# Optimization experiments

Measured on AMD Instinct MI355X. Metric: run time of the kernel, lower is better.

The kernel has to match this reference:

```python
import jax, jax.numpy as jnp
import numpy as np

B, N, F, T, K, FO = 16, 1024, 64, 24, 3, 64


def setup_inputs() -> dict:
    key = jax.random.key(0)
    ks = jax.random.split(key, 8)
    sc = 0.05
    x = jax.random.normal(ks[0], (B, N, F, T), dtype=jnp.float32)
    W1 = jax.random.normal(ks[1], (T,), dtype=jnp.float32) * sc
    W2 = jax.random.normal(ks[2], (F, T), dtype=jnp.float32) * sc
    W3 = jax.random.normal(ks[3], (F,), dtype=jnp.float32) * sc
    bs = jax.random.normal(ks[4], (1, N, N), dtype=jnp.float32) * sc
    Vs = jax.random.normal(ks[5], (N, N), dtype=jnp.float32) * sc
    cheb = jax.random.normal(ks[6], (K, N, N), dtype=jnp.float32) * sc
    Theta = jax.random.normal(ks[7], (K, F, FO), dtype=jnp.float32) * sc
    return {"x": x, "W1": W1, "W2": W2, "W3": W3, "bs": bs, "Vs": Vs,
            "cheb": cheb, "Theta": Theta}


def spatial_attention(x, W1, W2, W3, bs, Vs):
    # x: (B,N,F,T) -> S: (B,N,N)
    lhs = jnp.einsum('bnft,t->bnf', x, W1)          # (B,N,F)
    lhs = jnp.einsum('bnf,ft->bnt', lhs, W2)        # (B,N,T)
    rhs = jnp.einsum('f,bnft->btn', W3, x)          # (B,T,N)
    product = jnp.einsum('bnt,btm->bnm', lhs, rhs)  # (B,N,N)
    S = jnp.einsum('ik,bkj->bij', Vs, jax.nn.sigmoid(product + bs))
    return jax.nn.softmax(S, axis=1)


def reference(x, W1, W2, W3, bs, Vs, cheb, Theta):
    # x: (B,N,F,T); cheb: (K,N,N); Theta: (K,F,FO)
    S = spatial_attention(x, W1, W2, W3, bs, Vs)    # (B,N,N)
    out = jnp.zeros((x.shape[0], x.shape[1], Theta.shape[2], x.shape[3]),
                    dtype=x.dtype)
    for k in range(cheb.shape[0]):                  # small fixed K
        Tat = cheb[k] * S                           # (B,N,N) attention-masked T_k
        # T_k_with_at.permute(0,2,1) @ graph_signal, vectorized over t
        r = jnp.einsum('bnm,bnft->bmft', Tat, x)    # (B,N,F,T)
        out = out + jnp.einsum('bmft,fo->bmot', r, Theta[k])
    return jax.nn.relu(out)                         # (B,N,FO,T)
```

## Files before the change

### kernel.cpp

```cpp
#include <hip/hip_runtime.h>
#include <math.h>

#define Bc 16
#define Nc 1024
#define Fc 64
#define Tc 24
#define Kc 3
#define FOc 64
#define Cc (Fc*Tc)
#define KKc (Kc*Nc)

typedef __attribute__((ext_vector_type(8))) short short8;
typedef __attribute__((ext_vector_type(8))) unsigned short u16x8;
typedef __attribute__((ext_vector_type(4))) float f32x4;

__device__ __forceinline__ unsigned short f2bf(float f) {
  unsigned u = __float_as_uint(f);
  u += 0x7fff + ((u >> 16) & 1);
  return (unsigned short)(u >> 16);
}
__device__ __forceinline__ float bf2f(unsigned short h) {
  return __uint_as_float((unsigned)h << 16);
}

#define GLL16(g, l) __builtin_amdgcn_global_load_lds( \
    (const __attribute__((address_space(1))) void*)(g), \
    (__attribute__((address_space(3))) void*)(l), 16, 0, 0)

__device__ __forceinline__ f32x4 mfma16(short8 a, short8 b, f32x4 c) {
  return __builtin_amdgcn_mfma_f32_16x16x32_bf16(a, b, c, 0, 0, 0);
}

__global__ __launch_bounds__(64) void prep_kernel(
    const float* __restrict__ x, const float* __restrict__ W1,
    const float* __restrict__ W2, const float* __restrict__ W3,
    float* __restrict__ lhs, float* __restrict__ rhs) {
  int bn = blockIdx.x;
  int tid = threadIdx.x;
  __shared__ float xs[Fc * 25];
  __shared__ float w1s[Tc];
  __shared__ float w3s[Fc];
  __shared__ float af[Fc];
  const float* xp = x + (size_t)bn * Cc;
  for (int i = tid; i < Cc; i += 64) xs[(i / Tc) * 25 + (i % Tc)] = xp[i];
  if (tid < Tc) w1s[tid] = W1[tid];
  w3s[tid] = W3[tid];
  __syncthreads();
  float a = 0.f;
  #pragma unroll
  for (int t = 0; t < Tc; ++t) a += xs[tid * 25 + t] * w1s[t];
  af[tid] = a;
  __syncthreads();
  if (tid < Tc) {
    float l = 0.f, r2 = 0.f;
    #pragma unroll 8
    for (int f = 0; f < Fc; ++f) {
      l  += af[f] * W2[f * Tc + tid];
      r2 += w3s[f] * xs[f * 25 + tid];
    }
    lhs[(size_t)bn * Tc + tid] = l;
    rhs[(size_t)bn * Tc + tid] = r2;
  }
}

__global__ __launch_bounds__(256) void prodsigT_kernel(
    const float* __restrict__ lhs, const float* __restrict__ rhs,
    const float* __restrict__ bs, unsigned short* __restrict__ sigT) {
  int b = blockIdx.z;
  int p0 = blockIdx.y * 64, q0 = blockIdx.x * 64;
  __shared__ float Ls[64 * 25], Rs[64 * 25], Bt[64 * 65];
  int tid = threadIdx.x;
  const float* lp = lhs + ((size_t)b * Nc + q0) * Tc;
  const float* rp = rhs + ((size_t)b * Nc + p0) * Tc;
  for (int i = tid; i < 64 * Tc; i += 256) {
    Ls[(i / Tc) * 25 + i % Tc] = lp[i];
    Rs[(i / Tc) * 25 + i % Tc] = rp[i];
  }
  for (int i = tid; i < 1024; i += 256) {
    int qr = i >> 4, pc = (i & 15) * 4;
    *(float4*)&Bt[qr * 65 + pc] = *(const float4*)&bs[(size_t)(q0 + qr) * Nc + p0 + pc];
  }
  __syncthreads();
  int tx = tid % 16, ty = tid / 16;
  float acc[4][4] = {};
  for (int t = 0; t < Tc; ++t) {
    float rv[4], lv[4];
    #pragma unroll
    for (int i = 0; i < 4; ++i) rv[i] = Rs[(ty * 4 + i) * 25 + t];
    #pragma unroll
    for (int j = 0; j < 4; ++j) lv[j] = Ls[(tx * 4 + j) * 25 + t];
    #pragma unroll
    for (int i = 0; i < 4; ++i)
      #pragma unroll
      for (int j = 0; j < 4; ++j) acc[i][j] += rv[i] * lv[j];
  }
  #pragma unroll
  for (int i = 0; i < 4; ++i) {
    int p = p0 + ty * 4 + i;
    ushort4 o;
    float v0 = acc[i][0] + Bt[(tx * 4 + 0) * 65 + ty * 4 + i];
    float v1 = acc[i][1] + Bt[(tx * 4 + 1) * 65 + ty * 4 + i];
    float v2 = acc[i][2] + Bt[(tx * 4 + 2) * 65 + ty * 4 + i];
    float v3 = acc[i][3] + Bt[(tx * 4 + 3) * 65 + ty * 4 + i];
    o.x = f2bf(1.f / (1.f + __expf(-v0)));
    o.y = f2bf(1.f / (1.f + __expf(-v1)));
    o.z = f2bf(1.f / (1.f + __expf(-v2)));
    o.w = f2bf(1.f / (1.f + __expf(-v3)));
    *(ushort4*)&sigT[((size_t)b * Nc + p) * Nc + q0 + tx * 4] = o;
  }
}

__global__ __launch_bounds__(256) void cvt_vs_kernel(
    const float* __restrict__ Vs, unsigned short* __restrict__ Vsbf) {
  int i = (blockIdx.x * 256 + threadIdx.x) * 4;
  float4 v = *(const float4*)&Vs[i];
  ushort4 o;
  o.x = f2bf(v.x); o.y = f2bf(v.y); o.z = f2bf(v.z); o.w = f2bf(v.w);
  *(ushort4*)&Vsbf[i] = o;
}

__global__ __launch_bounds__(256) void chebT_kernel(
    const float* __restrict__ cheb, float* __restrict__ chebT) {
  int k = blockIdx.z;
  int n0 = blockIdx.y * 64, m0 = blockIdx.x * 64;
  __shared__ float t[64 * 65];
  const float* src = cheb + (size_t)k * Nc * Nc;
  float* dst = chebT + (size_t)k * Nc * Nc;
  int tid = threadIdx.x;
  #pragma unroll
  for (int s = 0; s < 4; ++s) {
    int nr = (tid >> 4) + s * 16, mc = (tid & 15) * 4;
    float4 v = *(const float4*)&src[(size_t)(n0 + nr) * Nc + m0 + mc];
    t[(mc + 0) * 65 + nr] = v.x;
    t[(mc + 1) * 65 + nr] = v.y;
    t[(mc + 2) * 65 + nr] = v.z;
    t[(mc + 3) * 65 + nr] = v.w;
  }
  __syncthreads();
  #pragma unroll
  for (int s = 0; s < 4; ++s) {
    int mr = (tid >> 4) + s * 16, nc = (tid & 15) * 4;
    float4 v = {t[mr * 65 + nc], t[mr * 65 + nc + 1], t[mr * 65 + nc + 2], t[mr * 65 + nc + 3]};
    *(float4*)&dst[(size_t)(m0 + mr) * Nc + n0 + nc] = v;
  }
}

__global__ __launch_bounds__(256) void xt2_kernel(
    const float* __restrict__ x, unsigned short* __restrict__ xt2) {
  __shared__ unsigned short ld[4 * Cc];
  int w = threadIdx.x >> 6, lane = threadIdx.x & 63;
  size_t n = (size_t)blockIdx.x * 4 + w;
  const float* xp = x + n * Cc;
  unsigned short* op = xt2 + n * Cc;
  #pragma unroll
  for (int j = 0; j < 24; ++j) {
    int i = j * 64 + lane;
    int f = i / 24, t = i - f * 24;
    ld[w * Cc + t * 64 + f] = f2bf(xp[i]);
  }
  __syncthreads();
  #pragma unroll
  for (int j = 0; j < 24; ++j)
    op[j * 64 + lane] = ld[w * Cc + j * 64 + lane];
}

__global__ __launch_bounds__(256) void tcat_kernel(
    const float* __restrict__ Theta, unsigned short* __restrict__ tcat) {
  int i = blockIdx.x * 256 + threadIdx.x;
  int m2 = i >> 6, f = i & 63;
  int k = m2 >> 6, o = m2 & 63;
  tcat[i] = (m2 < 192) ? f2bf(Theta[((size_t)k * Fc + f) * FOc + o])
                       : (unsigned short)0;
}

__global__ __launch_bounds__(256) void softmax_rows_kernel(unsigned short* __restrict__ ST) {
  int row = (blockIdx.x * 256 + threadIdx.x) >> 6;
  int lane = threadIdx.x & 63;
  unsigned short* rp = ST + (size_t)row * Nc + lane * 16;
  u16x8 r0 = *(const u16x8*)rp;
  u16x8 r1 = *(const u16x8*)(rp + 8);
  float v[16];
  #pragma unroll
  for (int s = 0; s < 8; ++s) { v[s] = bf2f(r0[s]); v[8 + s] = bf2f(r1[s]); }
  float m = -INFINITY;
  #pragma unroll
  for (int s = 0; s < 16; ++s) m = fmaxf(m, v[s]);
  #pragma unroll
  for (int off = 32; off; off >>= 1) m = fmaxf(m, __shfl_xor(m, off));
  float sum = 0.f;
  #pragma unroll
  for (int s = 0; s < 16; ++s) { v[s] = __expf(v[s] - m); sum += v[s]; }
  #pragma unroll
  for (int off = 32; off; off >>= 1) sum += __shfl_xor(sum, off);
  float inv = 1.f / sum;
  #pragma unroll
  for (int s = 0; s < 8; ++s) { r0[s] = f2bf(v[s] * inv); r1[s] = f2bf(v[8 + s] * inv); }
  *(u16x8*)rp = r0;
  *(u16x8*)(rp + 8) = r1;
}

__global__ __launch_bounds__(256) void maskcat_kernel(
    const float* __restrict__ chebT, const unsigned short* __restrict__ ST,
    unsigned short* __restrict__ Acat, int bbase) {
  int tg = blockIdx.x * 256 + threadIdx.x;
  int n0 = (tg & 127) * 8;
  int m  = (tg >> 7) & 1023;
  int bl = tg >> 17;
  const unsigned short* sp = ST + ((size_t)(bbase + bl) * Nc + m) * Nc + n0;
  u16x8 s = *(const u16x8*)sp;
  float sv[8];
  #pragma unroll
  for (int e = 0; e < 8; ++e) sv[e] = bf2f(s[e]);
  unsigned short* ap = Acat + ((size_t)bl * Nc + m) * KKc + n0;
  #pragma unroll
  for (int k = 0; k < Kc; ++k) {
    const float* cp = chebT + ((size_t)k * Nc + m) * Nc + n0;
    float4 c0 = *(const float4*)cp;
    float4 c1 = *(const float4*)(cp + 4);
    u16x8 o;
    o[0] = f2bf(c0.x * sv[0]);
    o[1] = f2bf(c0.y * sv[1]);
    o[2] = f2bf(c0.z * sv[2]);
    o[3] = f2bf(c0.w * sv[3]);
    o[4] = f2bf(c1.x * sv[4]);
    o[5] = f2bf(c1.y * sv[5]);
    o[6] = f2bf(c1.z * sv[6]);
    o[7] = f2bf(c1.w * sv[7]);
    *(u16x8*)(ap + k * Nc) = o;
  }
}

template <int MODE>
__global__ __launch_bounds__(256) void mfma_gemm_bt(
    const unsigned short* __restrict__ A, const unsigned short* __restrict__ B,
    void* __restrict__ Cv, int K, int CN,
    long long Abatch, long long Bbatch, long long Cbatch) {
  __shared__ unsigned short As[128 * 32];
  __shared__ unsigned short Bs[128 * 32];
  int b = blockIdx.z;
  int tid = threadIdx.x;
  int wave = tid >> 6, lane = tid & 63;
  const unsigned short* Ag = A + (size_t)b * Abatch + (size_t)blockIdx.y * 128 * K;
  const unsigned short* Bg = B + (size_t)b * Bbatch + (size_t)blockIdx.x * 128 * K;
  int srow = wave * 32 + (lane >> 2);
  int scol = (lane & 3) * 8;
  const unsigned short* ag0 = Ag + (size_t)srow * K + scol;
  const unsigned short* ag1 = ag0 + (size_t)16 * K;
  const unsigned short* bg0 = Bg + (size_t)srow * K + scol;
  const unsigned short* bg1 = bg0 + (size_t)16 * K;
  unsigned short* as0 = As + (wave * 32) * 32;
  unsigned short* as1 = As + (wave * 32 + 16) * 32;
  unsigned short* bs0 = Bs + (wave * 32) * 32;
  unsigned short* bs1 = Bs + (wave * 32 + 16) * 32;
  int rw = (wave >> 1) * 64, cw = (wave & 1) * 64;
  int frow = lane & 15, fk = (lane >> 4) * 8;
  f32x4 zero = {0.f, 0.f, 0.f, 0.f};
  f32x4 acc[4][4];
  #pragma unroll
  for (int i = 0; i < 4; ++i)
    #pragma unroll
    for (int j = 0; j < 4; ++j) acc[i][j] = zero;

  for (int k0 = 0; k0 < K; k0 += 32) {
    GLL16(ag0, as0); GLL16(ag1, as1);
    GLL16(bg0, bs0); GLL16(bg1, bs1);
    ag0 += 32; ag1 += 32; bg0 += 32; bg1 += 32;
    __syncthreads();
    short8 afr[4], bfr[4];
    #pragma unroll
    for (int i = 0; i < 4; ++i)
      afr[i] = *(const short8*)&As[(rw + i * 16 + frow) * 32 + fk];
    #pragma unroll
    for (int j = 0; j < 4; ++j)
      bfr[j] = *(const short8*)&Bs[(cw + j * 16 + frow) * 32 + fk];
    #pragma unroll
    for (int i = 0; i < 4; ++i)
      #pragma unroll
      for (int j = 0; j < 4; ++j)
        acc[i][j] = mfma16(afr[i], bfr[j], acc[i][j]);
    __syncthreads();
  }
  int q = lane >> 4, cl = lane & 15;
  if (MODE == 0) {
    unsigned short* Cg = (unsigned short*)Cv + (size_t)b * Cbatch
                         + (size_t)blockIdx.y * 128 * CN + (size_t)blockIdx.x * 128;
    #pragma unroll
    for (int i = 0; i < 4; ++i)
      #pragma unroll
      for (int j = 0; j < 4; ++j)
        #pragma unroll
        for (int e = 0; e < 4; ++e)
          Cg[(size_t)(rw + i * 16 + q * 4 + e) * CN + cw + j * 16 + cl] =
              f2bf(acc[i][j][e]);
  } else {
    float* Cg = (float*)Cv + (size_t)b * Cbatch
                + (size_t)blockIdx.y * 128 * CN + (size_t)blockIdx.x * 128;
    #pragma unroll
    for (int i = 0; i < 4; ++i)
      #pragma unroll
      for (int j = 0; j < 4; ++j)
        #pragma unroll
        for (int e = 0; e < 4; ++e)
          Cg[(size_t)(rw + i * 16 + q * 4 + e) * CN + cw + j * 16 + cl] =
              fmaxf(acc[i][j][e], 0.f);
  }
}

__global__ __launch_bounds__(256) void y2_gemm(
    const unsigned short* __restrict__ tcat, const unsigned short* __restrict__ xt2,
    unsigned short* __restrict__ ycat, int bbase) {
  __shared__ unsigned short As[128 * 32];
  __shared__ unsigned short Bs[128 * 32];
  int z = blockIdx.z;
  int bl = z / 24, t = z - bl * 24;
  int tid = threadIdx.x, wave = tid >> 6, lane = tid & 63;
  const unsigned short* Ag = tcat + (size_t)blockIdx.y * 128 * 64;
  const unsigned short* Bg = xt2 + ((size_t)(bbase + bl) * Nc + (size_t)blockIdx.x * 128) * Cc
                             + (size_t)t * 64;
  int srow = wave * 32 + (lane >> 2);
  int scol = (lane & 3) * 8;
  const unsigned short* ag0 = Ag + (size_t)srow * 64 + scol;
  const unsigned short* ag1 = ag0 + (size_t)16 * 64;
  const unsigned short* bg0 = Bg + (size_t)srow * Cc + scol;
  const unsigned short* bg1 = bg0 + (size_t)16 * Cc;
  unsigned short* as0 = As + (wave * 32) * 32;
  unsigned short* as1 = As + (wave * 32 + 16) * 32;
  unsigned short* bs0 = Bs + (wave * 32) * 32;
  unsigned short* bs1 = Bs + (wave * 32 + 16) * 32;
  int rw = (wave >> 1) * 64, cw = (wave & 1) * 64;
  int frow = lane & 15, fk = (lane >> 4) * 8;
  f32x4 zero = {0.f, 0.f, 0.f, 0.f};
  f32x4 acc[4][4];
  #pragma unroll
  for (int i = 0; i < 4; ++i)
    #pragma unroll
    for (int j = 0; j < 4; ++j) acc[i][j] = zero;

  for (int k0 = 0; k0 < 64; k0 += 32) {
    GLL16(ag0, as0); GLL16(ag1, as1);
    GLL16(bg0, bs0); GLL16(bg1, bs1);
    ag0 += 32; ag1 += 32; bg0 += 32; bg1 += 32;
    __syncthreads();
    short8 afr[4], bfr[4];
    #pragma unroll
    for (int i = 0; i < 4; ++i)
      afr[i] = *(const short8*)&As[(rw + i * 16 + frow) * 32 + fk];
    #pragma unroll
    for (int j = 0; j < 4; ++j)
      bfr[j] = *(const short8*)&Bs[(cw + j * 16 + frow) * 32 + fk];
    #pragma unroll
    for (int i = 0; i < 4; ++i)
      #pragma unroll
      for (int j = 0; j < 4; ++j)
        acc[i][j] = mfma16(afr[i], bfr[j], acc[i][j]);
    __syncthreads();
  }
  int q = lane >> 4, cl = lane & 15;
  unsigned short* yb = ycat + (size_t)bl * Cc * KKc + (size_t)t * KKc;
  #pragma unroll
  for (int i = 0; i < 4; ++i)
    #pragma unroll
    for (int e = 0; e < 4; ++e) {
      int m2 = blockIdx.y * 128 + rw + i * 16 + q * 4 + e;
      if (m2 < 192) {
        int kk = m2 >> 6, o = m2 & 63;
        unsigned short* dst = yb + (size_t)o * 24 * KKc + kk * Nc;
        #pragma unroll
        for (int j = 0; j < 4; ++j)
          dst[blockIdx.x * 128 + cw + j * 16 + cl] = f2bf(acc[i][j][e]);
      }
    }
}

extern "C" void kernel_launch(void* const* d_in, const int* in_sizes, int n_in,
                              void* d_out, int out_size, void* d_ws, size_t ws_size,
                              hipStream_t stream) {
  const float* x     = (const float*)d_in[0];
  const float* W1    = (const float*)d_in[1];
  const float* W2    = (const float*)d_in[2];
  const float* W3    = (const float*)d_in[3];
  const float* bs    = (const float*)d_in[4];
  const float* Vs    = (const float*)d_in[5];
  const float* cheb  = (const float*)d_in[6];
  const float* Theta = (const float*)d_in[7];
  float* out = (float*)d_out;

  char* w = (char*)d_ws;
  unsigned short* ycat = (unsigned short*)w;
  float* lhs = (float*)w;
  float* rhs = (float*)(w + 1572864);
  unsigned short* sigT = (unsigned short*)(w + 3145728);
  unsigned short* Vsbf = (unsigned short*)(w + 36700160);
  unsigned short* Acat = (unsigned short*)(w + 75497472);
  unsigned short* ST   = (unsigned short*)(w + 125829120);
  float* chebT         = (float*)(w + 159383552);
  unsigned short* xt2  = (unsigned short*)(w + 171966464);
  unsigned short* tcat = (unsigned short*)(w + 222298112);

  prep_kernel<<<Bc * Nc, 64, 0, stream>>>(x, W1, W2, W3, lhs, rhs);
  prodsigT_kernel<<<dim3(Nc / 64, Nc / 64, Bc), 256, 0, stream>>>(lhs, rhs, bs, sigT);
  cvt_vs_kernel<<<Nc * Nc / 1024, 256, 0, stream>>>(Vs, Vsbf);
  mfma_gemm_bt<0><<<dim3(Nc / 128, Nc / 128, Bc), 256, 0, stream>>>(
      sigT, Vsbf, ST, Nc, Nc, (long long)Nc * Nc, 0LL, (long long)Nc * Nc);
  softmax_rows_kernel<<<Bc * Nc / 4, 256, 0, stream>>>(ST);
  chebT_kernel<<<dim3(Nc / 64, Nc / 64, Kc), 256, 0, stream>>>(cheb, chebT);
  xt2_kernel<<<Bc * Nc / 4, 256, 0, stream>>>(x, xt2);
  tcat_kernel<<<64, 256, 0, stream>>>(Theta, tcat);

  for (int half = 0; half < 2; ++half) {
    int bbase = half * 8;
    maskcat_kernel<<<4096, 256, 0, stream>>>(chebT, ST, Acat, bbase);
    y2_gemm<<<dim3(Nc / 128, 2, 8 * 24), 256, 0, stream>>>(tcat, xt2, ycat, bbase);
    mfma_gemm_bt<1><<<dim3(Cc / 128, Nc / 128, 8), 256, 0, stream>>>(
        Acat, ycat, out + (size_t)bbase * Nc * Cc, KKc, Cc,
        (long long)Nc * KKc, (long long)Cc * KKc, (long long)Nc * Cc);
  }
}
```

Measured before the change: 659.8 us.

## Fuse x prep kernels, fold softmax into masking, widen GEMM K-tile with swizzle

Merges the lhs/rhs projection kernel and the bf16 transpose of x into one kernel that reads x once. Folds the row softmax into the cheb-masking kernel, which removes a separate read-modify-write pass over ST. Replaces the duplicated GEMM main loops with a shared core that uses a 64-wide K tile and an XOR-swizzled LDS layout, halving barrier count and reducing bank conflicts. The wider tile doubles LDS use per block, which may lower occupancy.

```diff
diff --git a/kernel.cpp b/kernel.cpp
--- a/kernel.cpp
+++ b/kernel.cpp
@@ -31,35 +31,84 @@
   return __builtin_amdgcn_mfma_f32_16x16x32_bf16(a, b, c, 0, 0, 0);
 }
 
-__global__ __launch_bounds__(64) void prep_kernel(
+__device__ __forceinline__ void gemm_core(
+    const unsigned short* __restrict__ Ag, const unsigned short* __restrict__ Bg,
+    int lda, int ldb, int K,
+    unsigned short* As, unsigned short* Bs,
+    int wave, int lane, f32x4 acc[4][4]) {
+  int sr = lane >> 3;
+  int sc = ((lane & 7) ^ sr) * 8;
+  const unsigned short* a0 = Ag + (size_t)(wave * 32 + sr) * lda + sc;
+  const unsigned short* b0 = Bg + (size_t)(wave * 32 + sr) * ldb + sc;
+  unsigned short* asw = As + (wave * 32) * 64;
+  unsigned short* bsw = Bs + (wave * 32) * 64;
+  int rw = (wave >> 1) * 64, cw = (wave & 1) * 64;
+  int frow = lane & 15;
+  int q = lane >> 4;
+  int p0 = (q ^ (frow & 7)) * 8;
+  int p1 = ((q | 4) ^ (frow & 7)) * 8;
+  for (int k0 = 0; k0 < K; k0 += 64) {
+    #pragma unroll
+    for (int c = 0; c < 4; ++c) {
+      GLL16(a0 + (size_t)(c * 8) * lda + k0, asw + (c * 8) * 64);
+      GLL16(b0 + (size_t)(c * 8) * ldb + k0, bsw + (c * 8) * 64);
+    }
+    __syncthreads();
+    #pragma unroll
+    for (int h = 0; h < 2; ++h) {
+      int p = h ? p1 : p0;
+      short8 afr[4], bfr[4];
+      #pragma unroll
+      for (int i = 0; i < 4; ++i)
+        afr[i] = *(const short8*)&As[(rw + i * 16 + frow) * 64 + p];
+      #pragma unroll
+      for (int j = 0; j < 4; ++j)
+        bfr[j] = *(const short8*)&Bs[(cw + j * 16 + frow) * 64 + p];
+      #pragma unroll
+      for (int i = 0; i < 4; ++i)
+        #pragma unroll
+        for (int j = 0; j < 4; ++j)
+          acc[i][j] = mfma16(afr[i], bfr[j], acc[i][j]);
+    }
+    __syncthreads();
+  }
+}
+
+__global__ __launch_bounds__(256) void xprep_kernel(
     const float* __restrict__ x, const float* __restrict__ W1,
     const float* __restrict__ W2, const float* __restrict__ W3,
-    float* __restrict__ lhs, float* __restrict__ rhs) {
-  int bn = blockIdx.x;
-  int tid = threadIdx.x;
-  __shared__ float xs[Fc * 25];
-  __shared__ float w1s[Tc];
-  __shared__ float w3s[Fc];
-  __shared__ float af[Fc];
-  const float* xp = x + (size_t)bn * Cc;
-  for (int i = tid; i < Cc; i += 64) xs[(i / Tc) * 25 + (i % Tc)] = xp[i];
-  if (tid < Tc) w1s[tid] = W1[tid];
-  w3s[tid] = W3[tid];
+    unsigned short* __restrict__ xt2, float* __restrict__ lhs,
+    float* __restrict__ rhs) {
+  __shared__ float ld[4 * 1560];
+  __shared__ float af[4 * 64];
+  int w = threadIdx.x >> 6, lane = threadIdx.x & 63;
+  size_t n = (size_t)blockIdx.x * 4 + w;
+  const float* xp = x + n * Cc;
+  float* lw = ld + w * 1560;
+  #pragma unroll
+  for (int j = 0; j < 24; ++j) {
+    int i = j * 64 + lane;
+    int f = i / 24, t = i - f * 24;
+    lw[t * 65 + f] = xp[i];
+  }
   __syncthreads();
   float a = 0.f;
   #pragma unroll
-  for (int t = 0; t < Tc; ++t) a += xs[tid * 25 + t] * w1s[t];
-  af[tid] = a;
-  __syncthreads();
-  if (tid < Tc) {
-    float l = 0.f, r2 = 0.f;
+  for (int t = 0; t < Tc; ++t) a += lw[t * 65 + lane] * W1[t];
+  af[w * 64 + lane] = a;
+  #pragma unroll
+  for (int j = 0; j < 24; ++j)
+    xt2[n * Cc + j * 64 + lane] = f2bf(lw[j * 65 + lane]);
+  __syncthreads();
+  if (lane < Tc) {
+    float l = 0.f, r = 0.f;
     #pragma unroll 8
     for (int f = 0; f < Fc; ++f) {
-      l  += af[f] * W2[f * Tc + tid];
-      r2 += w3s[f] * xs[f * 25 + tid];
+      l += af[w * 64 + f] * W2[f * Tc + lane];
+      r += W3[f] * lw[lane * 65 + f];
     }
-    lhs[(size_t)bn * Tc + tid] = l;
-    rhs[(size_t)bn * Tc + tid] = r2;
+    lhs[n * Tc + lane] = l;
+    rhs[n * Tc + lane] = r;
   }
 }
 
@@ -145,25 +194,6 @@
   }
 }
 
-__global__ __launch_bounds__(256) void xt2_kernel(
-    const float* __restrict__ x, unsigned short* __restrict__ xt2) {
-  __shared__ unsigned short ld[4 * Cc];
-  int w = threadIdx.x >> 6, lane = threadIdx.x & 63;
-  size_t n = (size_t)blockIdx.x * 4 + w;
-  const float* xp = x + n * Cc;
-  unsigned short* op = xt2 + n * Cc;
-  #pragma unroll
-  for (int j = 0; j < 24; ++j) {
-    int i = j * 64 + lane;
-    int f = i / 24, t = i - f * 24;
-    ld[w * Cc + t * 64 + f] = f2bf(xp[i]);
-  }
-  __syncthreads();
-  #pragma unroll
-  for (int j = 0; j < 24; ++j)
-    op[j * 64 + lane] = ld[w * Cc + j * 64 + lane];
-}
-
 __global__ __launch_bounds__(256) void tcat_kernel(
     const float* __restrict__ Theta, unsigned short* __restrict__ tcat) {
   int i = blockIdx.x * 256 + threadIdx.x;
@@ -173,60 +203,40 @@
                        : (unsigned short)0;
 }
 
-__global__ __launch_bounds__(256) void softmax_rows_kernel(unsigned short* __restrict__ ST) {
-  int row = (blockIdx.x * 256 + threadIdx.x) >> 6;
-  int lane = threadIdx.x & 63;
-  unsigned short* rp = ST + (size_t)row * Nc + lane * 16;
-  u16x8 r0 = *(const u16x8*)rp;
-  u16x8 r1 = *(const u16x8*)(rp + 8);
-  float v[16];
-  #pragma unroll
-  for (int s = 0; s < 8; ++s) { v[s] = bf2f(r0[s]); v[8 + s] = bf2f(r1[s]); }
-  float m = -INFINITY;
-  #pragma unroll
-  for (int s = 0; s < 16; ++s) m = fmaxf(m, v[s]);
-  #pragma unroll
-  for (int off = 32; off; off >>= 1) m = fmaxf(m, __shfl_xor(m, off));
-  float sum = 0.f;
-  #pragma unroll
-  for (int s = 0; s < 16; ++s) { v[s] = __expf(v[s] - m); sum += v[s]; }
-  #pragma unroll
-  for (int off = 32; off; off >>= 1) sum += __shfl_xor(sum, off);
-  float inv = 1.f / sum;
-  #pragma unroll
-  for (int s = 0; s < 8; ++s) { r0[s] = f2bf(v[s] * inv); r1[s] = f2bf(v[8 + s] * inv); }
-  *(u16x8*)rp = r0;
-  *(u16x8*)(rp + 8) = r1;
-}
-
-__global__ __launch_bounds__(256) void maskcat_kernel(
+__global__ __launch_bounds__(256) void masksoft_kernel(
     const float* __restrict__ chebT, const unsigned short* __restrict__ ST,
     unsigned short* __restrict__ Acat, int bbase) {
-  int tg = blockIdx.x * 256 + threadIdx.x;
-  int n0 = (tg & 127) * 8;
-  int m  = (tg >> 7) & 1023;
-  int bl = tg >> 17;
-  const unsigned short* sp = ST + ((size_t)(bbase + bl) * Nc + m) * Nc + n0;
-  u16x8 s = *(const u16x8*)sp;
-  float sv[8];
-  #pragma unroll
-  for (int e = 0; e < 8; ++e) sv[e] = bf2f(s[e]);
-  unsigned short* ap = Acat + ((size_t)bl * Nc + m) * KKc + n0;
+  int m  = blockIdx.x & (Nc - 1);
+  int bl = blockIdx.x >> 10;
+  int tid = threadIdx.x;
+  const unsigned short* sp = ST + ((size_t)(bbase + bl) * Nc + m) * Nc;
+  ushort4 s4 = *(const ushort4*)(sp + tid * 4);
+  float v0 = bf2f(s4.x), v1 = bf2f(s4.y), v2 = bf2f(s4.z), v3 = bf2f(s4.w);
+  __shared__ float redm[4], reds[4];
+  int wave = tid >> 6, lane = tid & 63;
+  float mx = fmaxf(fmaxf(v0, v1), fmaxf(v2, v3));
+  #pragma unroll
+  for (int off = 32; off; off >>= 1) mx = fmaxf(mx, __shfl_xor(mx, off));
+  if (lane == 0) redm[wave] = mx;
+  __syncthreads();
+  mx = fmaxf(fmaxf(redm[0], redm[1]), fmaxf(redm[2], redm[3]));
+  float e0 = __expf(v0 - mx), e1 = __expf(v1 - mx);
+  float e2 = __expf(v2 - mx), e3 = __expf(v3 - mx);
+  float sm = e0 + e1 + e2 + e3;
+  #pragma unroll
+  for (int off = 32; off; off >>= 1) sm += __shfl_xor(sm, off);
+  if (lane == 0) reds[wave] = sm;
+  __syncthreads();
+  float inv = 1.f / (reds[0] + reds[1] + reds[2] + reds[3]);
+  e0 *= inv; e1 *= inv; e2 *= inv; e3 *= inv;
+  unsigned short* ap = Acat + ((size_t)bl * Nc + m) * KKc + tid * 4;
   #pragma unroll
   for (int k = 0; k < Kc; ++k) {
-    const float* cp = chebT + ((size_t)k * Nc + m) * Nc + n0;
-    float4 c0 = *(const float4*)cp;
-    float4 c1 = *(const float4*)(cp + 4);
-    u16x8 o;
-    o[0] = f2bf(c0.x * sv[0]);
-    o[1] = f2bf(c0.y * sv[1]);
-    o[2] = f2bf(c0.z * sv[2]);
-    o[3] = f2bf(c0.w * sv[3]);
-    o[4] = f2bf(c1.x * sv[4]);
-    o[5] = f2bf(c1.y * sv[5]);
-    o[6] = f2bf(c1.z * sv[6]);
-    o[7] = f2bf(c1.w * sv[7]);
-    *(u16x8*)(ap + k * Nc) = o;
+    float4 c = *(const float4*)&chebT[((size_t)k * Nc + m) * Nc + tid * 4];
+    ushort4 o;
+    o.x = f2bf(c.x * e0); o.y = f2bf(c.y * e1);
+    o.z = f2bf(c.z * e2); o.w = f2bf(c.w * e3);
+    *(ushort4*)(ap + k * Nc) = o;
   }
 }
 
@@ -235,51 +245,20 @@
     const unsigned short* __restrict__ A, const unsigned short* __restrict__ B,
     void* __restrict__ Cv, int K, int CN,
     long long Abatch, long long Bbatch, long long Cbatch) {
-  __shared__ unsigned short As[128 * 32];
-  __shared__ unsigned short Bs[128 * 32];
+  __shared__ unsigned short As[128 * 64];
+  __shared__ unsigned short Bs[128 * 64];
   int b = blockIdx.z;
-  int tid = threadIdx.x;
-  int wave = tid >> 6, lane = tid & 63;
+  int tid = threadIdx.x, wave = tid >> 6, lane = tid & 63;
   const unsigned short* Ag = A + (size_t)b * Abatch + (size_t)blockIdx.y * 128 * K;
   const unsigned short* Bg = B + (size_t)b * Bbatch + (size_t)blockIdx.x * 128 * K;
-  int srow = wave * 32 + (lane >> 2);
-  int scol = (lane & 3) * 8;
-  const unsigned short* ag0 = Ag + (size_t)srow * K + scol;
-  const unsigned short* ag1 = ag0 + (size_t)16 * K;
-  const unsigned short* bg0 = Bg + (size_t)srow * K + scol;
-  const unsigned short* bg1 = bg0 + (size_t)16 * K;
-  unsigned short* as0 = As + (wave * 32) * 32;
-  unsigned short* as1 = As + (wave * 32 + 16) * 32;
-  unsigned short* bs0 = Bs + (wave * 32) * 32;
-  unsigned short* bs1 = Bs + (wave * 32 + 16) * 32;
-  int rw = (wave >> 1) * 64, cw = (wave & 1) * 64;
-  int frow = lane & 15, fk = (lane >> 4) * 8;
   f32x4 zero = {0.f, 0.f, 0.f, 0.f};
   f32x4 acc[4][4];
   #pragma unroll
   for (int i = 0; i < 4; ++i)
     #pragma unroll
     for (int j = 0; j < 4; ++j) acc[i][j] = zero;
-
-  for (int k0 = 0; k0 < K; k0 += 32) {
-    GLL16(ag0, as0); GLL16(ag1, as1);
-    GLL16(bg0, bs0); GLL16(bg1, bs1);
-    ag0 += 32; ag1 += 32; bg0 += 32; bg1 += 32;
-    __syncthreads();
-    short8 afr[4], bfr[4];
-    #pragma unroll
-    for (int i = 0; i < 4; ++i)
-      afr[i] = *(const short8*)&As[(rw + i * 16 + frow) * 32 + fk];
-    #pragma unroll
-    for (int j = 0; j < 4; ++j)
-      bfr[j] = *(const short8*)&Bs[(cw + j * 16 + frow) * 32 + fk];
-    #pragma unroll
-    for (int i = 0; i < 4; ++i)
-      #pragma unroll
-      for (int j = 0; j < 4; ++j)
-        acc[i][j] = mfma16(afr[i], bfr[j], acc[i][j]);
-    __syncthreads();
-  }
+  gemm_core(Ag, Bg, K, K, K, As, Bs, wave, lane, acc);
+  int rw = (wave >> 1) * 64, cw = (wave & 1) * 64;
   int q = lane >> 4, cl = lane & 15;
   if (MODE == 0) {
     unsigned short* Cg = (unsigned short*)Cv + (size_t)b * Cbatch
@@ -309,52 +288,22 @@
 __global__ __launch_bounds__(256) void y2_gemm(
     const unsigned short* __restrict__ tcat, const unsigned short* __restrict__ xt2,
     unsigned short* __restrict__ ycat, int bbase) {
-  __shared__ unsigned short As[128 * 32];
-  __shared__ unsigned short Bs[128 * 32];
+  __shared__ unsigned short As[128 * 64];
+  __shared__ unsigned short Bs[128 * 64];
   int z = blockIdx.z;
   int bl = z / 24, t = z - bl * 24;
   int tid = threadIdx.x, wave = tid >> 6, lane = tid & 63;
   const unsigned short* Ag = tcat + (size_t)blockIdx.y * 128 * 64;
   const unsigned short* Bg = xt2 + ((size_t)(bbase + bl) * Nc + (size_t)blockIdx.x * 128) * Cc
                              + (size_t)t * 64;
-  int srow = wave * 32 + (lane >> 2);
-  int scol = (lane & 3) * 8;
-  const unsigned short* ag0 = Ag + (size_t)srow * 64 + scol;
-  const unsigned short* ag1 = ag0 + (size_t)16 * 64;
-  const unsigned short* bg0 = Bg + (size_t)srow * Cc + scol;
-  const unsigned short* bg1 = bg0 + (size_t)16 * Cc;
-  unsigned short* as0 = As + (wave * 32) * 32;
-  unsigned short* as1 = As + (wave * 32 + 16) * 32;
-  unsigned short* bs0 = Bs + (wave * 32) * 32;
-  unsigned short* bs1 = Bs + (wave * 32 + 16) * 32;
-  int rw = (wave >> 1) * 64, cw = (wave & 1) * 64;
-  int frow = lane & 15, fk = (lane >> 4) * 8;
   f32x4 zero = {0.f, 0.f, 0.f, 0.f};
   f32x4 acc[4][4];
   #pragma unroll
   for (int i = 0; i < 4; ++i)
     #pragma unroll
     for (int j = 0; j < 4; ++j) acc[i][j] = zero;
-
-  for (int k0 = 0; k0 < 64; k0 += 32) {
-    GLL16(ag0, as0); GLL16(ag1, as1);
-    GLL16(bg0, bs0); GLL16(bg1, bs1);
-    ag0 += 32; ag1 += 32; bg0 += 32; bg1 += 32;
-    __syncthreads();
-    short8 afr[4], bfr[4];
-    #pragma unroll
-    for (int i = 0; i < 4; ++i)
-      afr[i] = *(const short8*)&As[(rw + i * 16 + frow) * 32 + fk];
-    #pragma unroll
-    for (int j = 0; j < 4; ++j)
-      bfr[j] = *(const short8*)&Bs[(cw + j * 16 + frow) * 32 + fk];
-    #pragma unroll
-    for (int i = 0; i < 4; ++i)
-      #pragma unroll
-      for (int j = 0; j < 4; ++j)
-        acc[i][j] = mfma16(afr[i], bfr[j], acc[i][j]);
-    __syncthreads();
-  }
+  gemm_core(Ag, Bg, 64, Cc, 64, As, Bs, wave, lane, acc);
+  int rw = (wave >> 1) * 64, cw = (wave & 1) * 64;
   int q = lane >> 4, cl = lane & 15;
   unsigned short* yb = ycat + (size_t)bl * Cc * KKc + (size_t)t * KKc;
   #pragma unroll
@@ -397,19 +346,17 @@
   unsigned short* xt2  = (unsigned short*)(w + 171966464);
   unsigned short* tcat = (unsigned short*)(w + 222298112);
 
-  prep_kernel<<<Bc * Nc, 64, 0, stream>>>(x, W1, W2, W3, lhs, rhs);
+  xprep_kernel<<<Bc * Nc / 4, 256, 0, stream>>>(x, W1, W2, W3, xt2, lhs, rhs);
   prodsigT_kernel<<<dim3(Nc / 64, Nc / 64, Bc), 256, 0, stream>>>(lhs, rhs, bs, sigT);
   cvt_vs_kernel<<<Nc * Nc / 1024, 256, 0, stream>>>(Vs, Vsbf);
   mfma_gemm_bt<0><<<dim3(Nc / 128, Nc / 128, Bc), 256, 0, stream>>>(
       sigT, Vsbf, ST, Nc, Nc, (long long)Nc * Nc, 0LL, (long long)Nc * Nc);
-  softmax_rows_kernel<<<Bc * Nc / 4, 256, 0, stream>>>(ST);
   chebT_kernel<<<dim3(Nc / 64, Nc / 64, Kc), 256, 0, stream>>>(cheb, chebT);
-  xt2_kernel<<<Bc * Nc / 4, 256, 0, stream>>>(x, xt2);
   tcat_kernel<<<64, 256, 0, stream>>>(Theta, tcat);
 
   for (int half = 0; half < 2; ++half) {
     int bbase = half * 8;
-    maskcat_kernel<<<4096, 256, 0, stream>>>(chebT, ST, Acat, bbase);
+    masksoft_kernel<<<8 * Nc, 256, 0, stream>>>(chebT, ST, Acat, bbase);
     y2_gemm<<<dim3(Nc / 128, 2, 8 * 24), 256, 0, stream>>>(tcat, xt2, ycat, bbase);
     mfma_gemm_bt<1><<<dim3(Cc / 128, Nc / 128, 8), 256, 0, stream>>>(
         Acat, ycat, out + (size_t)bbase * Nc * Cc, KKc, Cc,
```

After: 566.5 us. 14.1% less time.
